# Optimization experiments

Hardware: AMD Instinct MI355X
Metric: run time of the kernel (lower is better)

The kernel has to match this reference:

```python
import jax, jax.numpy as jnp
import numpy as np
import math

EPS = 1e-6
NOISE = 1e-5

def _icnn(x, w0r, b0, w1r, b1, zw, g0r, g1r, ob):
    # x: [..., D]; returns [..., P, D]
    w0 = jax.nn.softplus(w0r) ** 2            # [P, 2D, D]
    w1 = jax.nn.softplus(w1r) ** 2            # [P, D, 2D]
    g0 = jax.nn.sigmoid(g0r)[:, None]          # [P, 1]
    g1 = jax.nn.sigmoid(g1r)[:, None]
    z0 = jax.nn.softplus((jnp.einsum('...d,pkd->...pk', x, w0) + b0) * g0)  # [..., P, 2D]
    xw1 = jnp.einsum('...pk,pdk->...pd', z0, w1) + b1                        # [..., P, D]
    zmap = jnp.einsum('...pk,pkd->...pd', z0, zw)
    z1 = jax.nn.softplus(xw1 * g1 + zmap)
    return z1 + ob

def _convex_gate(x, gw, gb):
    u = jax.nn.softplus(jnp.einsum('...d,od->...o', x, gw) + gb)
    return 1.0 - jnp.exp(-u)  # [..., 1]

def _scalar_hull(x, w0r, b0, w1r, b1, zw, g0r, g1r, ob, gw, gb, key):
    g = _convex_gate(x, gw, gb)
    xg = (x + jax.random.normal(key, x.shape, x.dtype) * NOISE) * g
    r = jnp.sqrt(jnp.mean(xg * xg, axis=-1, keepdims=True) + EPS)
    tau = jnp.exp(0.30343 * r + 0.22159)
    scores = _icnn(xg, w0r, b0, w1r, b1, zw, g0r, g1r, ob).mean(-1)  # [..., P]
    lse = jax.nn.logsumexp(scores * tau, axis=-1, keepdims=True)
    return jnp.squeeze(lse / tau, -1)

def _mixer(q, k, v, mask, qp, kp, whq, whk):
    keys = jax.random.split(jax.random.key(42), 6)
    gate_q = jax.nn.softplus(q)
    q = q * gate_q
    r = jnp.sqrt(jnp.mean(q * q, axis=-1, keepdims=True) + EPS)  # [B,H,S,1]
    tau = jnp.exp(0.30343 * r + 0.22159)
    fq = _scalar_hull(q, *qp, keys[0])  # [B,H,S]
    gk = _scalar_hull(k, *kp, keys[1])
    # creative: perturbed dual evaluations, detached delta
    qn = (jax.random.uniform(keys[2], q.shape, q.dtype) - 0.5) * NOISE
    kn = (jax.random.uniform(keys[3], k.shape, k.dtype) - 0.5) * NOISE
    fq_ = _scalar_hull(q + qn, *qp, keys[4])
    gk_ = _scalar_hull(k + kn, *kp, keys[5])
    fq = fq - 0.1 * jax.lax.stop_gradient(fq_ - fq)
    gk = gk - 0.1 * jax.lax.stop_gradient(gk_ - gk)
    phi_q = jax.nn.softplus(jnp.minimum(jnp.einsum('bhsd,rd->bhsr', q, whq), 20.0))
    phi_k = jax.nn.softplus(jnp.minimum(jnp.einsum('bhsd,rd->bhsr', k, whk), 20.0))
    # LSE_r(log(phi_q+eps) + log(phi_k+eps)) == log((phi_q+eps) @ (phi_k+eps)^T), exactly
    logK = jnp.log(jnp.einsum('bhir,bhjr->bhij', phi_q + EPS, phi_k + EPS))
    scores = fq[..., None] + gk[..., None, :] + logK + jnp.log(jnp.maximum(mask, EPS))
    logits = scores * tau  # tau [B,H,S,1] broadcasts over keys
    log_w = logits - jax.nn.logsumexp(logits, axis=-1, keepdims=True)
    w = jnp.exp(log_w)
    out = jnp.einsum('bhij,bhjd->bhid', w, v)
    a = jax.nn.softmax(w.sum(-3), axis=-1).mean(1)  # [B, S]
    mn = a.min(-1, keepdims=True)
    mx = a.max(-1, keepdims=True)
    a = (a - mn) / (mx - mn + EPS)
    return out, a

def setup_inputs() -> dict:
    B, H, S, D, P, R = 2, 8, 1024, 64, 8, 16
    d1 = 2 * D
    key = jax.random.key(0)
    ks = jax.random.split(key, 32)
    mean0 = math.log(math.sqrt(2.0 / D))
    mean1 = math.log(math.sqrt(2.0 / d1))
    def hull_params(i):
        kk = jax.random.split(ks[i], 6)
        return dict(
            w0=mean0 + 0.2 * jax.random.normal(kk[0], (P, d1, D)),
            b0=jnp.zeros((P, d1)),
            w1=mean1 + 0.2 * jax.random.normal(kk[1], (P, D, d1)),
            b1=jnp.zeros((P, D)),
            zw=jax.random.uniform(kk[2], (P, d1, D), minval=-1.0, maxval=1.0) / math.sqrt(d1 * D) * math.sqrt(6.0),
            g0=jnp.full((P,), -3.0),
            g1=jnp.full((P,), -3.0),
            ob=jnp.zeros((P, D)),
            gw=jax.random.normal(kk[3], (1, D)) / math.sqrt(D),
            gb=jnp.zeros((1,)),
        )
    qp = hull_params(10)
    kp = hull_params(11)
    inp = {
        'q': jax.random.normal(ks[0], (B, H, S, D)),
        'k': jax.random.normal(ks[1], (B, H, S, D)),
        'v': jax.random.normal(ks[2], (B, H, S, D)),
        'mask': jax.random.uniform(ks[3], (B, H, S, S)),
        'whq': jax.random.normal(ks[4], (R, D)) / math.sqrt(D),
        'whk': jax.random.normal(ks[5], (R, D)) / math.sqrt(D),
    }
    for name, p in (('q', qp), ('k', kp)):
        for pn, pv in p.items():
            inp[f'{name}_{pn}'] = pv
    return inp

def reference(q, k, v, mask,
              q_w0, q_b0, q_w1, q_b1, q_zw, q_g0, q_g1, q_ob, q_gw, q_gb,
              k_w0, k_b0, k_w1, k_b1, k_zw, k_g0, k_g1, k_ob, k_gw, k_gb,
              whq, whk):
    qp = (q_w0, q_b0, q_w1, q_b1, q_zw, q_g0, q_g1, q_ob, q_gw, q_gb)
    kp = (k_w0, k_b0, k_w1, k_b1, k_zw, k_g0, k_g1, k_ob, k_gw, k_gb)
    return _mixer(q, k, v, mask, qp, kp, whq, whk)
```

## Files before the change

### kernel.cpp

```cpp
#include <hip/hip_runtime.h>
#include <hip/hip_bf16.h>
#include <math.h>

typedef __hip_bfloat16 bf16;
typedef __attribute__((ext_vector_type(8))) short short8;
typedef __attribute__((ext_vector_type(4))) float f32x4;
#define EPSF 1e-6f

__device__ __forceinline__ float b2f(bf16 v){ return __bfloat162float(v); }
__device__ __forceinline__ bf16  f2b(float v){ return __float2bfloat16(v); }
__device__ __forceinline__ float spf(float x){ return x > 20.f ? x : __logf(1.f + __expf(x)); }
__device__ __forceinline__ float sigf(float x){ return 1.f/(1.f + __expf(-x)); }

__device__ __forceinline__ float wsum(float v){
#pragma unroll
  for (int m = 32; m; m >>= 1) v += __shfl_xor(v, m, 64);
  return v;
}
__device__ __forceinline__ float wmaxr(float v){
#pragma unroll
  for (int m = 32; m; m >>= 1) v = fmaxf(v, __shfl_xor(v, m, 64));
  return v;
}
__device__ __forceinline__ float wminr(float v){
#pragma unroll
  for (int m = 32; m; m >>= 1) v = fminf(v, __shfl_xor(v, m, 64));
  return v;
}
__device__ __forceinline__ void unp(float fv, float& lo, float& hi){
  unsigned u = __float_as_uint(fv);
  lo = __uint_as_float(u << 16);
  hi = __uint_as_float(u & 0xffff0000u);
}

struct PrepArgs {
  const float* w0r[2]; const float* b0[2]; const float* w1r[2]; const float* b1[2];
  const float* zw[2];  const float* g0[2]; const float* g1[2]; const float* ob[2];
  bf16* W0gB[2]; bf16* MtB[2]; float* b0g[2]; float* B1g[2]; float* obm[2];
};

__global__ __launch_bounds__(256) void prep_kernel(PrepArgs a){
  int idx = blockIdx.x*256 + threadIdx.x;
  int s = idx >> 16, r = idx & 65535;
  {
    int p = r >> 13;
    float g0 = sigf(a.g0[s][p]);
    float w  = spf(a.w0r[s][r]);
    a.W0gB[s][r] = f2b(g0 * w * w);
  }
  {
    int pd = r >> 7, kk = r & 127;
    int p = pd >> 6, d = pd & 63;
    float g1 = sigf(a.g1[s][p]);
    float w  = spf(a.w1r[s][r]);
    float z  = a.zw[s][(p<<13) + (kk<<6) + d];
    a.MtB[s][r] = f2b(g1 * w * w + z);
  }
  if (r < 1024) a.b0g[s][r] = sigf(a.g0[s][r>>7]) * a.b0[s][r];
  if (r < 512)  a.B1g[s][r] = sigf(a.g1[s][r>>6]) * a.b1[s][r];
  if (r < 8) {
    float t = 0.f;
    for (int d = 0; d < 64; ++d) t += a.ob[s][r*64 + d];
    a.obm[s][r] = t * (1.f/64.f);
  }
}

__global__ __launch_bounds__(256) void vprep_kernel(const float* __restrict__ v, bf16* __restrict__ vT){
  __shared__ float vL[64][65];
  int bh = blockIdx.x >> 4, jt = blockIdx.x & 15;
  int j0 = jt * 64, t = threadIdx.x;
  for (int i = 0; i < 16; ++i) {
    int idx = t + i*256;
    int jj = idx >> 6, d = idx & 63;
    vL[jj][d] = v[((long)bh*1024 + j0 + jj)*64 + d];
  }
  __syncthreads();
  for (int i = 0; i < 16; ++i) {
    int idx = t + i*256;
    int dd = idx >> 6, js = idx & 63;
    vT[((long)bh*64 + dd)*1024 + j0 + js] = f2b(vL[js][dd]);
  }
}

struct HullArgs {
  const float* x[2]; const float* gw[2]; const float* gb[2]; const float* wh[2];
  const bf16* W0gB[2]; const bf16* MtB[2];
  const float* b0g[2]; const float* B1g[2]; const float* obm[2];
  float* tauOut; float* fOut[2]; float* phiOut[2];
};

__global__ __launch_bounds__(256) void hull_kernel(HullArgs A){
  __shared__ __align__(16) bf16 xgb[16][72];
  __shared__ __align__(16) bf16 z0[16][1032];
  __shared__ float tauh[16];
  __shared__ float scoreb[16][8];
  int bid = blockIdx.x;
  int s = bid >> 10;
  int isQ = (s == 0);
  long row0 = (long)(bid & 1023) * 16;
  const float* x   = A.x[s];
  const float* gw  = A.gw[s];
  const float* wh  = A.wh[s];
  const bf16* W0gB = A.W0gB[s];
  const bf16* MtB  = A.MtB[s];
  const float* b0g = A.b0g[s];
  const float* B1g = A.B1g[s];
  const float* obm = A.obm[s];
  float* fOut   = A.fOut[s];
  float* phiOut = A.phiOut[s];
  int t = threadIdx.x, lane = t & 63, w = t >> 6;
  float gbf = A.gb[s][0];

  for (int rp = 0; rp < 4; ++rp) {
    int r = rp*4 + w;
    long row = row0 + r;
    float xv = x[row*64 + lane];
    float xh = isQ ? xv * spf(xv) : xv;
    float s1 = wsum(xh * gw[lane]);
    float g = 1.f - __expf(-spf(s1 + gbf));
    float xgv = xh * g;
    float msq = wsum(xgv*xgv)*(1.f/64.f) + EPSF;
    float th = __expf(0.30343f*sqrtf(msq) + 0.22159f);
    if (lane == 0) tauh[r] = th;
    if (isQ) {
      float m2 = wsum(xh*xh)*(1.f/64.f) + EPSF;
      if (lane == 0) A.tauOut[row] = __expf(0.30343f*sqrtf(m2) + 0.22159f);
    }
    xgb[r][lane] = f2b(xgv);
    float myphi = 0.f;
#pragma unroll
    for (int jj = 0; jj < 16; ++jj) {
      float pv = wsum(xh * wh[jj*64 + lane]);
      if (lane == jj) myphi = pv;
    }
    if (lane < 16) phiOut[row*16 + lane] = spf(fminf(myphi, 20.f)) + EPSF;
  }
  __syncthreads();

  {
    int g = lane >> 4, cl = lane & 15;
    short8 a0 = *(const short8*)&xgb[cl][g*8];
    short8 a1 = *(const short8*)&xgb[cl][32 + g*8];
    for (int ct = 0; ct < 16; ++ct) {
      int col = w*256 + ct*16 + cl;
      const short8* bp = (const short8*)(W0gB + col*64);
      short8 b0 = bp[g];
      short8 b1 = bp[4 + g];
      f32x4 acc = {0.f, 0.f, 0.f, 0.f};
      acc = __builtin_amdgcn_mfma_f32_16x16x32_bf16(a0, b0, acc, 0, 0, 0);
      acc = __builtin_amdgcn_mfma_f32_16x16x32_bf16(a1, b1, acc, 0, 0, 0);
      float bb = b0g[col];
#pragma unroll
      for (int rg = 0; rg < 4; ++rg)
        z0[g*4 + rg][col] = f2b(spf(acc[rg] + bb));
    }
  }
  __syncthreads();

  {
    int g = lane >> 4, cl = lane & 15;
    for (int pi = 0; pi < 2; ++pi) {
      int p = w + pi*4;
      short8 af[4];
#pragma unroll
      for (int kc = 0; kc < 4; ++kc)
        af[kc] = *(const short8*)&z0[cl][p*128 + kc*32 + g*8];
      float s0 = 0.f, s1 = 0.f, s2 = 0.f, s3 = 0.f;
#pragma unroll
      for (int nt = 0; nt < 4; ++nt) {
        int dcol = nt*16 + cl;
        const short8* mp = (const short8*)(MtB + (p*64 + dcol)*128);
        f32x4 acc = {0.f, 0.f, 0.f, 0.f};
#pragma unroll
        for (int kc = 0; kc < 4; ++kc)
          acc = __builtin_amdgcn_mfma_f32_16x16x32_bf16(af[kc], mp[kc*4 + g], acc, 0, 0, 0);
        float bb = B1g[p*64 + dcol];
        s0 += spf(acc[0] + bb);
        s1 += spf(acc[1] + bb);
        s2 += spf(acc[2] + bb);
        s3 += spf(acc[3] + bb);
      }
#pragma unroll
      for (int m = 1; m < 16; m <<= 1) {
        s0 += __shfl_xor(s0, m, 64);
        s1 += __shfl_xor(s1, m, 64);
        s2 += __shfl_xor(s2, m, 64);
        s3 += __shfl_xor(s3, m, 64);
      }
      if (cl == 0) {
        scoreb[g*4+0][p] = s0 * (1.f/64.f);
        scoreb[g*4+1][p] = s1 * (1.f/64.f);
        scoreb[g*4+2][p] = s2 * (1.f/64.f);
        scoreb[g*4+3][p] = s3 * (1.f/64.f);
      }
    }
  }
  __syncthreads();

  if (t < 16) {
    int r = t;
    float th = tauh[r];
    float li[8]; float m = -1e30f;
#pragma unroll
    for (int p = 0; p < 8; ++p) { li[p] = (scoreb[r][p] + obm[p]) * th; m = fmaxf(m, li[p]); }
    float ssum = 0.f;
#pragma unroll
    for (int p = 0; p < 8; ++p) ssum += __expf(li[p] - m);
    fOut[row0 + r] = (m + __logf(ssum)) / th;
  }
}

__global__ __launch_bounds__(512) void attn5_kernel(
  const float* __restrict__ mask, const bf16* __restrict__ vT,
  const float* __restrict__ phiQ, const float* __restrict__ phiK,
  const float* __restrict__ fqA, const float* __restrict__ gkA, const float* __restrict__ tauA,
  float* __restrict__ smPart0, float* __restrict__ smPart1, float* __restrict__ outO)
{
  __shared__ __align__(16) bf16 ebf[16][1032];
  __shared__ __align__(16) float smp[8][1024];
  __shared__ float phq[8][16];
  __shared__ float fqs[8], taus[8], sinvL[8];
  int t = threadIdx.x, lane = t & 63, w = t >> 6;
  int b = blockIdx.x >> 8, hg = (blockIdx.x >> 7) & 1, it = blockIdx.x & 127;
  int i0 = it * 8;

  {
    float* z = (float*)&ebf[8][0];
    for (int idx = t; idx < 4128; idx += 512) z[idx] = 0.f;
  }

  for (int h = 0; h < 4; ++h) {
    int bh = b*8 + hg*4 + h;
    long pbase = (long)bh * 1024;
    if (t < 128) { int r = t >> 4, c = t & 15;
      phq[r][c] = phiQ[(pbase + i0 + r)*16 + c]; }
    else if (t < 136) { int r = t - 128; fqs[r] = fqA[pbase + i0 + r]; }
    else if (t < 144) { int r = t - 136; taus[r] = tauA[pbase + i0 + r]; }
    __syncthreads();

    float l[16];
    {
      float pq[16];
#pragma unroll
      for (int c = 0; c < 16; ++c) pq[c] = phq[w][c];
      float fq = fqs[w], ta = taus[w];
      const float* pkb = phiK + pbase*16;
      const float* mrow = mask + (pbase + i0 + w)*1024;
      const float* gkb = gkA + pbase;
#pragma unroll 2
      for (int c = 0; c < 16; ++c) {
        int j = c*64 + lane;
        const float4* pk = (const float4*)(pkb + j*16);
        float4 k0 = pk[0], k1 = pk[1], k2 = pk[2], k3 = pk[3];
        float dp = pq[0]*k0.x + pq[1]*k0.y + pq[2]*k0.z + pq[3]*k0.w
                 + pq[4]*k1.x + pq[5]*k1.y + pq[6]*k1.z + pq[7]*k1.w
                 + pq[8]*k2.x + pq[9]*k2.y + pq[10]*k2.z + pq[11]*k2.w
                 + pq[12]*k3.x + pq[13]*k3.y + pq[14]*k3.z + pq[15]*k3.w;
        float mk = fmaxf(mrow[j], EPSF);
        l[c] = (fq + gkb[j] + __logf(dp * mk)) * ta;
      }
    }
    {
      float m = -1e30f;
#pragma unroll
      for (int c = 0; c < 16; ++c) m = fmaxf(m, l[c]);
      m = wmaxr(m);
      float s = 0.f;
#pragma unroll
      for (int c = 0; c < 16; ++c) {
        float e = __expf(l[c] - m);
        s += e;
        ebf[w][c*64 + lane] = f2b(e);
      }
      s = wsum(s);
      if (lane == 0) sinvL[w] = 1.f / s;
    }
    __syncthreads();

    if (w < 4) {
      int g = lane >> 4, cl = lane & 15;
      const short8* bp = (const short8*)(vT + ((long)bh*64 + w*16 + cl)*1024);
      f32x4 cf = {0.f, 0.f, 0.f, 0.f};
      for (int kc = 0; kc < 32; ++kc) {
        short8 aF = *(const short8*)&ebf[cl][kc*32 + g*8];
        short8 bF = bp[kc*4 + g];
        cf = __builtin_amdgcn_mfma_f32_16x16x32_bf16(aF, bF, cf, 0, 0, 0);
      }
      if (g < 2) {
#pragma unroll
        for (int i = 0; i < 4; ++i) {
          int row = g*4 + i;
          outO[(pbase + i0 + row)*64 + w*16 + cl] = cf[i] * sinvL[row];
        }
      }
    } else {
      int r0 = (w-4)*2;
#pragma unroll
      for (int rr = 0; rr < 2; ++rr) {
        int r = r0 + rr;
        float sv = sinvL[r];
#pragma unroll
        for (int ch = 0; ch < 4; ++ch) {
          int jb = ch*256 + lane*4;
          uint2 eb = *(const uint2*)&ebf[r][jb];
          float e0,e1,e2,e3;
          unp(__uint_as_float(eb.x), e0, e1);
          unp(__uint_as_float(eb.y), e2, e3);
          float4 acc;
          if (h == 0) acc = make_float4(0.f,0.f,0.f,0.f);
          else        acc = *(float4*)&smp[r][jb];
          acc.x += sv*e0; acc.y += sv*e1; acc.z += sv*e2; acc.w += sv*e3;
          *(float4*)&smp[r][jb] = acc;
        }
      }
    }
    __syncthreads();
  }

  {
    float* dst = (hg == 0 ? smPart0 : smPart1) + ((long)b*1024 + i0)*1024;
    for (int idx = t; idx < 2048; idx += 512) {
      int r = idx >> 8, j4 = (idx & 255)*4;
      *(float4*)&dst[(long)r*1024 + j4] = *(const float4*)&smp[r][j4];
    }
  }
}

__global__ __launch_bounds__(256) void smsoft_kernel(
  const float* __restrict__ p0, const float* __restrict__ p1, float* __restrict__ aAcc)
{
  int b = blockIdx.x >> 7, ii = blockIdx.x & 127;
  int t = threadIdx.x, lane = t & 63, w = t >> 6;
  __shared__ float redm[4], reds[4];
  float a0 = 0.f, a1 = 0.f, a2 = 0.f, a3 = 0.f;
  for (int i = 0; i < 8; ++i) {
    long row = ((long)b*1024 + ii*8 + i)*1024 + t*4;
    float4 v0 = *(const float4*)(p0 + row);
    float4 v1 = *(const float4*)(p1 + row);
    float4 v = make_float4(v0.x+v1.x, v0.y+v1.y, v0.z+v1.z, v0.w+v1.w);
    float m = fmaxf(fmaxf(v.x, v.y), fmaxf(v.z, v.w));
    m = wmaxr(m);
    if (lane == 0) redm[w] = m;
    __syncthreads();
    m = fmaxf(fmaxf(redm[0], redm[1]), fmaxf(redm[2], redm[3]));
    float4 e;
    e.x = __expf(v.x - m); e.y = __expf(v.y - m); e.z = __expf(v.z - m); e.w = __expf(v.w - m);
    float s = e.x + e.y + e.z + e.w;
    s = wsum(s);
    if (lane == 0) reds[w] = s;
    __syncthreads();
    s = reds[0] + reds[1] + reds[2] + reds[3];
    float inv = 1.f / (s * 1024.f);
    a0 += e.x*inv; a1 += e.y*inv; a2 += e.z*inv; a3 += e.w*inv;
    __syncthreads();
  }
  atomicAdd(&aAcc[b*1024 + t*4+0], a0);
  atomicAdd(&aAcc[b*1024 + t*4+1], a1);
  atomicAdd(&aAcc[b*1024 + t*4+2], a2);
  atomicAdd(&aAcc[b*1024 + t*4+3], a3);
}

__global__ __launch_bounds__(1024) void anorm_kernel(const float* __restrict__ aAcc, float* __restrict__ outA){
  int b = blockIdx.x, t = threadIdx.x, lane = t & 63, w = t >> 6;
  float v = aAcc[b*1024 + t];
  __shared__ float rmn[16], rmx[16];
  float mn = wminr(v), mx = wmaxr(v);
  if (lane == 0) { rmn[w] = mn; rmx[w] = mx; }
  __syncthreads();
  mn = rmn[0]; mx = rmx[0];
#pragma unroll
  for (int i = 1; i < 16; ++i) { mn = fminf(mn, rmn[i]); mx = fmaxf(mx, rmx[i]); }
  outA[b*1024 + t] = (v - mn) / (mx - mn + EPSF);
}

extern "C" void kernel_launch(void* const* d_in, const int* in_sizes, int n_in,
                              void* d_out, int out_size, void* d_ws, size_t ws_size,
                              hipStream_t stream)
{
  (void)in_sizes; (void)n_in; (void)out_size; (void)ws_size;
  const float* q    = (const float*)d_in[0];
  const float* k    = (const float*)d_in[1];
  const float* v    = (const float*)d_in[2];
  const float* mask = (const float*)d_in[3];
  const float* whq  = (const float*)d_in[4];
  const float* whk  = (const float*)d_in[5];

  float* ws = (float*)d_ws;
  bf16* w0b_q = (bf16*)(ws);
  bf16* w0b_k = (bf16*)(ws + 32768);
  bf16* mtb_q = (bf16*)(ws + 65536);
  bf16* mtb_k = (bf16*)(ws + 98304);
  float* b0g_q = ws + 131072;
  float* b0g_k = ws + 132096;
  float* B1g_q = ws + 133120;
  float* B1g_k = ws + 133632;
  float* obm_q = ws + 134144;
  float* obm_k = ws + 134160;
  float* tau_q = ws + 134176;
  float* fq_a  = ws + 150560;
  float* gk_a  = ws + 166944;
  float* phi_q = ws + 183328;
  float* phi_k = ws + 445472;
  bf16*  v_T   = (bf16*)(ws + 707616);
  float* a_acc = ws + 1231904;
  float* smP0  = ws + 1233952;
  float* smP1  = ws + 3331104;

  hipMemsetAsync(a_acc, 0, 2048*sizeof(float), stream);

  PrepArgs pa;
  for (int s = 0; s < 2; ++s) {
    int o = 6 + 10*s;
    pa.w0r[s] = (const float*)d_in[o+0];
    pa.b0 [s] = (const float*)d_in[o+1];
    pa.w1r[s] = (const float*)d_in[o+2];
    pa.b1 [s] = (const float*)d_in[o+3];
    pa.zw [s] = (const float*)d_in[o+4];
    pa.g0 [s] = (const float*)d_in[o+5];
    pa.g1 [s] = (const float*)d_in[o+6];
    pa.ob [s] = (const float*)d_in[o+7];
  }
  pa.W0gB[0]=w0b_q; pa.W0gB[1]=w0b_k; pa.MtB[0]=mtb_q; pa.MtB[1]=mtb_k;
  pa.b0g[0]=b0g_q; pa.b0g[1]=b0g_k; pa.B1g[0]=B1g_q; pa.B1g[1]=B1g_k;
  pa.obm[0]=obm_q; pa.obm[1]=obm_k;

  prep_kernel<<<512,256,0,stream>>>(pa);
  vprep_kernel<<<256,256,0,stream>>>(v, v_T);

  HullArgs ha;
  ha.x[0] = q; ha.x[1] = k;
  ha.gw[0] = (const float*)d_in[14]; ha.gw[1] = (const float*)d_in[24];
  ha.gb[0] = (const float*)d_in[15]; ha.gb[1] = (const float*)d_in[25];
  ha.wh[0] = whq; ha.wh[1] = whk;
  ha.W0gB[0] = w0b_q; ha.W0gB[1] = w0b_k;
  ha.MtB[0] = mtb_q;  ha.MtB[1] = mtb_k;
  ha.b0g[0] = b0g_q;  ha.b0g[1] = b0g_k;
  ha.B1g[0] = B1g_q;  ha.B1g[1] = B1g_k;
  ha.obm[0] = obm_q;  ha.obm[1] = obm_k;
  ha.tauOut = tau_q;
  ha.fOut[0] = fq_a;  ha.fOut[1] = gk_a;
  ha.phiOut[0] = phi_q; ha.phiOut[1] = phi_k;

  hull_kernel<<<2048,256,0,stream>>>(ha);

  attn5_kernel<<<512,512,0,stream>>>(mask, v_T, phi_q, phi_k, fq_a, gk_a, tau_q,
                                     smP0, smP1, (float*)d_out);
  smsoft_kernel<<<256,256,0,stream>>>(smP0, smP1, a_acc);
  anorm_kernel<<<2,1024,0,stream>>>(a_acc, (float*)d_out + 1048576);
}
```

Baseline: 220.5 us.

## Process 16 query rows per attention block and merge prep kernels

Each attention block now handles 16 query rows instead of 8. This fills all 16 MFMA rows, which were previously half zero-padded, and halves the number of times V and phiK are reloaded per row. The shared-memory softmax accumulator is dropped: each head's partial sums are read and written directly in the global partial buffers. The weight-prep and V-transpose kernels are merged into one launch. The trade-offs are half as many attention blocks, so less parallelism, and extra global read-modify-write traffic for the partial sums.

```diff
diff --git a/kernel.cpp b/kernel.cpp
--- a/kernel.cpp
+++ b/kernel.cpp
@@ -36,49 +36,53 @@
 struct PrepArgs {
   const float* w0r[2]; const float* b0[2]; const float* w1r[2]; const float* b1[2];
   const float* zw[2];  const float* g0[2]; const float* g1[2]; const float* ob[2];
+  const float* v;
   bf16* W0gB[2]; bf16* MtB[2]; float* b0g[2]; float* B1g[2]; float* obm[2];
+  bf16* vT;
 };
 
-__global__ __launch_bounds__(256) void prep_kernel(PrepArgs a){
-  int idx = blockIdx.x*256 + threadIdx.x;
-  int s = idx >> 16, r = idx & 65535;
-  {
-    int p = r >> 13;
-    float g0 = sigf(a.g0[s][p]);
-    float w  = spf(a.w0r[s][r]);
-    a.W0gB[s][r] = f2b(g0 * w * w);
-  }
-  {
-    int pd = r >> 7, kk = r & 127;
-    int p = pd >> 6, d = pd & 63;
-    float g1 = sigf(a.g1[s][p]);
-    float w  = spf(a.w1r[s][r]);
-    float z  = a.zw[s][(p<<13) + (kk<<6) + d];
-    a.MtB[s][r] = f2b(g1 * w * w + z);
-  }
-  if (r < 1024) a.b0g[s][r] = sigf(a.g0[s][r>>7]) * a.b0[s][r];
-  if (r < 512)  a.B1g[s][r] = sigf(a.g1[s][r>>6]) * a.b1[s][r];
-  if (r < 8) {
-    float t = 0.f;
-    for (int d = 0; d < 64; ++d) t += a.ob[s][r*64 + d];
-    a.obm[s][r] = t * (1.f/64.f);
-  }
-}
-
-__global__ __launch_bounds__(256) void vprep_kernel(const float* __restrict__ v, bf16* __restrict__ vT){
-  __shared__ float vL[64][65];
-  int bh = blockIdx.x >> 4, jt = blockIdx.x & 15;
-  int j0 = jt * 64, t = threadIdx.x;
-  for (int i = 0; i < 16; ++i) {
-    int idx = t + i*256;
-    int jj = idx >> 6, d = idx & 63;
-    vL[jj][d] = v[((long)bh*1024 + j0 + jj)*64 + d];
-  }
-  __syncthreads();
-  for (int i = 0; i < 16; ++i) {
-    int idx = t + i*256;
-    int dd = idx >> 6, js = idx & 63;
-    vT[((long)bh*64 + dd)*1024 + j0 + js] = f2b(vL[js][dd]);
+__global__ __launch_bounds__(256) void prepv_kernel(PrepArgs a){
+  int bid = blockIdx.x;
+  if (bid < 512) {
+    int idx = bid*256 + threadIdx.x;
+    int s = idx >> 16, r = idx & 65535;
+    {
+      int p = r >> 13;
+      float g0 = sigf(a.g0[s][p]);
+      float w  = spf(a.w0r[s][r]);
+      a.W0gB[s][r] = f2b(g0 * w * w);
+    }
+    {
+      int pd = r >> 7, kk = r & 127;
+      int p = pd >> 6, d = pd & 63;
+      float g1 = sigf(a.g1[s][p]);
+      float w  = spf(a.w1r[s][r]);
+      float z  = a.zw[s][(p<<13) + (kk<<6) + d];
+      a.MtB[s][r] = f2b(g1 * w * w + z);
+    }
+    if (r < 1024) a.b0g[s][r] = sigf(a.g0[s][r>>7]) * a.b0[s][r];
+    if (r < 512)  a.B1g[s][r] = sigf(a.g1[s][r>>6]) * a.b1[s][r];
+    if (r < 8) {
+      float t = 0.f;
+      for (int d = 0; d < 64; ++d) t += a.ob[s][r*64 + d];
+      a.obm[s][r] = t * (1.f/64.f);
+    }
+  } else {
+    __shared__ float vL[64][65];
+    int id2 = bid - 512;
+    int bh = id2 >> 4, jt = id2 & 15;
+    int j0 = jt * 64, t = threadIdx.x;
+    for (int i = 0; i < 16; ++i) {
+      int idx = t + i*256;
+      int jj = idx >> 6, d = idx & 63;
+      vL[jj][d] = a.v[((long)bh*1024 + j0 + jj)*64 + d];
+    }
+    __syncthreads();
+    for (int i = 0; i < 16; ++i) {
+      int idx = t + i*256;
+      int dd = idx >> 6, js = idx & 63;
+      a.vT[((long)bh*64 + dd)*1024 + j0 + js] = f2b(vL[js][dd]);
+    }
   }
 }
 
@@ -210,70 +214,69 @@
   }
 }
 
-__global__ __launch_bounds__(512) void attn5_kernel(
+__global__ __launch_bounds__(512) void attn6_kernel(
   const float* __restrict__ mask, const bf16* __restrict__ vT,
   const float* __restrict__ phiQ, const float* __restrict__ phiK,
   const float* __restrict__ fqA, const float* __restrict__ gkA, const float* __restrict__ tauA,
   float* __restrict__ smPart0, float* __restrict__ smPart1, float* __restrict__ outO)
 {
   __shared__ __align__(16) bf16 ebf[16][1032];
-  __shared__ __align__(16) float smp[8][1024];
-  __shared__ float phq[8][16];
-  __shared__ float fqs[8], taus[8], sinvL[8];
+  __shared__ float phq[16][16];
+  __shared__ float fqs[16], taus[16], sinvL[16];
   int t = threadIdx.x, lane = t & 63, w = t >> 6;
-  int b = blockIdx.x >> 8, hg = (blockIdx.x >> 7) & 1, it = blockIdx.x & 127;
-  int i0 = it * 8;
-
-  {
-    float* z = (float*)&ebf[8][0];
-    for (int idx = t; idx < 4128; idx += 512) z[idx] = 0.f;
-  }
+  int b = blockIdx.x >> 7, hg = (blockIdx.x >> 6) & 1, it = blockIdx.x & 63;
+  int i0 = it * 16;
+  float* smP = (hg == 0 ? smPart0 : smPart1) + ((long)b*1024 + i0)*1024;
 
   for (int h = 0; h < 4; ++h) {
     int bh = b*8 + hg*4 + h;
     long pbase = (long)bh * 1024;
-    if (t < 128) { int r = t >> 4, c = t & 15;
+    if (t < 256) { int r = t >> 4, c = t & 15;
       phq[r][c] = phiQ[(pbase + i0 + r)*16 + c]; }
-    else if (t < 136) { int r = t - 128; fqs[r] = fqA[pbase + i0 + r]; }
-    else if (t < 144) { int r = t - 136; taus[r] = tauA[pbase + i0 + r]; }
-    __syncthreads();
-
-    float l[16];
-    {
-      float pq[16];
-#pragma unroll
-      for (int c = 0; c < 16; ++c) pq[c] = phq[w][c];
-      float fq = fqs[w], ta = taus[w];
-      const float* pkb = phiK + pbase*16;
-      const float* mrow = mask + (pbase + i0 + w)*1024;
-      const float* gkb = gkA + pbase;
+    else if (t < 272) { int r = t - 256; fqs[r] = fqA[pbase + i0 + r]; }
+    else if (t < 288) { int r = t - 272; taus[r] = tauA[pbase + i0 + r]; }
+    __syncthreads();
+
+#pragma unroll
+    for (int rr = 0; rr < 2; ++rr) {
+      int row = w + rr*8;
+      float l[16];
+      {
+        float pq[16];
+#pragma unroll
+        for (int c = 0; c < 16; ++c) pq[c] = phq[row][c];
+        float fq = fqs[row], ta = taus[row];
+        const float* pkb = phiK + pbase*16;
+        const float* mrow = mask + (pbase + i0 + row)*1024;
+        const float* gkb = gkA + pbase;
 #pragma unroll 2
-      for (int c = 0; c < 16; ++c) {
-        int j = c*64 + lane;
-        const float4* pk = (const float4*)(pkb + j*16);
-        float4 k0 = pk[0], k1 = pk[1], k2 = pk[2], k3 = pk[3];
-        float dp = pq[0]*k0.x + pq[1]*k0.y + pq[2]*k0.z + pq[3]*k0.w
-                 + pq[4]*k1.x + pq[5]*k1.y + pq[6]*k1.z + pq[7]*k1.w
-                 + pq[8]*k2.x + pq[9]*k2.y + pq[10]*k2.z + pq[11]*k2.w
-                 + pq[12]*k3.x + pq[13]*k3.y + pq[14]*k3.z + pq[15]*k3.w;
-        float mk = fmaxf(mrow[j], EPSF);
-        l[c] = (fq + gkb[j] + __logf(dp * mk)) * ta;
-      }
-    }
-    {
-      float m = -1e30f;
-#pragma unroll
-      for (int c = 0; c < 16; ++c) m = fmaxf(m, l[c]);
-      m = wmaxr(m);
-      float s = 0.f;
-#pragma unroll
-      for (int c = 0; c < 16; ++c) {
-        float e = __expf(l[c] - m);
-        s += e;
-        ebf[w][c*64 + lane] = f2b(e);
-      }
-      s = wsum(s);
-      if (lane == 0) sinvL[w] = 1.f / s;
+        for (int c = 0; c < 16; ++c) {
+          int j = c*64 + lane;
+          const float4* pk = (const float4*)(pkb + j*16);
+          float4 k0 = pk[0], k1 = pk[1], k2 = pk[2], k3 = pk[3];
+          float dp = pq[0]*k0.x + pq[1]*k0.y + pq[2]*k0.z + pq[3]*k0.w
+                   + pq[4]*k1.x + pq[5]*k1.y + pq[6]*k1.z + pq[7]*k1.w
+                   + pq[8]*k2.x + pq[9]*k2.y + pq[10]*k2.z + pq[11]*k2.w
+                   + pq[12]*k3.x + pq[13]*k3.y + pq[14]*k3.z + pq[15]*k3.w;
+          float mk = fmaxf(mrow[j], EPSF);
+          l[c] = (fq + gkb[j] + __logf(dp * mk)) * ta;
+        }
+      }
+      {
+        float m = -1e30f;
+#pragma unroll
+        for (int c = 0; c < 16; ++c) m = fmaxf(m, l[c]);
+        m = wmaxr(m);
+        float s = 0.f;
+#pragma unroll
+        for (int c = 0; c < 16; ++c) {
+          float e = __expf(l[c] - m);
+          s += e;
+          ebf[row][c*64 + lane] = f2b(e);
+        }
+        s = wsum(s);
+        if (lane == 0) sinvL[row] = 1.f / s;
+      }
     }
     __syncthreads();
 
@@ -286,19 +289,18 @@
         short8 bF = bp[kc*4 + g];
         cf = __builtin_amdgcn_mfma_f32_16x16x32_bf16(aF, bF, cf, 0, 0, 0);
       }
-      if (g < 2) {
-#pragma unroll
-        for (int i = 0; i < 4; ++i) {
-          int row = g*4 + i;
-          outO[(pbase + i0 + row)*64 + w*16 + cl] = cf[i] * sinvL[row];
-        }
+#pragma unroll
+      for (int i = 0; i < 4; ++i) {
+        int row = g*4 + i;
+        outO[(pbase + i0 + row)*64 + w*16 + cl] = cf[i] * sinvL[row];
       }
     } else {
-      int r0 = (w-4)*2;
-#pragma unroll
-      for (int rr = 0; rr < 2; ++rr) {
+      int r0 = (w-4)*4;
+#pragma unroll
+      for (int rr = 0; rr < 4; ++rr) {
         int r = r0 + rr;
         float sv = sinvL[r];
+        float* dst = smP + (long)r*1024;
 #pragma unroll
         for (int ch = 0; ch < 4; ++ch) {
           int jb = ch*256 + lane*4;
@@ -308,21 +310,13 @@
           unp(__uint_as_float(eb.y), e2, e3);
           float4 acc;
           if (h == 0) acc = make_float4(0.f,0.f,0.f,0.f);
-          else        acc = *(float4*)&smp[r][jb];
+          else        acc = *(const float4*)&dst[jb];
           acc.x += sv*e0; acc.y += sv*e1; acc.z += sv*e2; acc.w += sv*e3;
-          *(float4*)&smp[r][jb] = acc;
+          *(float4*)&dst[jb] = acc;
         }
       }
     }
     __syncthreads();
-  }
-
-  {
-    float* dst = (hg == 0 ? smPart0 : smPart1) + ((long)b*1024 + i0)*1024;
-    for (int idx = t; idx < 2048; idx += 512) {
-      int r = idx >> 8, j4 = (idx & 255)*4;
-      *(float4*)&dst[(long)r*1024 + j4] = *(const float4*)&smp[r][j4];
-    }
   }
 }
 
@@ -420,12 +414,13 @@
     pa.g1 [s] = (const float*)d_in[o+6];
     pa.ob [s] = (const float*)d_in[o+7];
   }
+  pa.v = v;
   pa.W0gB[0]=w0b_q; pa.W0gB[1]=w0b_k; pa.MtB[0]=mtb_q; pa.MtB[1]=mtb_k;
   pa.b0g[0]=b0g_q; pa.b0g[1]=b0g_k; pa.B1g[0]=B1g_q; pa.B1g[1]=B1g_k;
   pa.obm[0]=obm_q; pa.obm[1]=obm_k;
-
-  prep_kernel<<<512,256,0,stream>>>(pa);
-  vprep_kernel<<<256,256,0,stream>>>(v, v_T);
+  pa.vT = v_T;
+
+  prepv_kernel<<<768,256,0,stream>>>(pa);
 
   HullArgs ha;
   ha.x[0] = q; ha.x[1] = k;
@@ -443,7 +438,7 @@
 
   hull_kernel<<<2048,256,0,stream>>>(ha);
 
-  attn5_kernel<<<512,512,0,stream>>>(mask, v_T, phi_q, phi_k, fq_a, gk_a, tau_q,
+  attn6_kernel<<<256,512,0,stream>>>(mask, v_T, phi_q, phi_k, fq_a, gk_a, tau_q,
                                      smP0, smP1, (float*)d_out);
   smsoft_kernel<<<256,256,0,stream>>>(smP0, smP1, a_acc);
   anorm_kernel<<<2,1024,0,stream>>>(a_acc, (float*)d_out + 1048576);
```

After: 219.2 us. Within noise of the previous version (-0.6%).
